# Kernel tuning notes

Measured on AMD Instinct MI355X. Metric: run time of the kernel, lower is better.

## Reference

```python
import jax, jax.numpy as jnp
import numpy as np
import math

B, S = 512, 100
L, U = 50000, 2000
D, LOC_DIM, USER_DIM, TEMP_DIM = 80, 56, 12, 12
NHEAD, DFF = 4, 160


def _pe(seq_len, d):
    pos = np.arange(seq_len, dtype=np.float32)[:, None]
    div = np.exp(np.arange(0, d, 2, dtype=np.float32) * (-math.log(10000.0) / d))
    pe = np.zeros((seq_len, d), dtype=np.float32)
    pe[:, 0::2] = np.sin(pos * div)
    pe[:, 1::2] = np.cos(pos * div)
    return jnp.asarray(pe)


def _ln(x, g, b, eps=1e-5):
    m = x.mean(-1, keepdims=True)
    v = ((x - m) ** 2).mean(-1, keepdims=True)
    return (x - m) * jax.lax.rsqrt(v + eps) * g + b


def setup_inputs():
    key = jax.random.key(0)
    ks = jax.random.split(key, 16)
    f32 = jnp.float32
    def n(k, shape, s):
        return (jax.random.normal(k, shape) * s).astype(f32)
    return {
        'loc_seq': jax.random.randint(ks[0], (B, S), 0, L),
        'user_seq': jax.random.randint(ks[1], (B, S), 0, U),
        'weekday_seq': jax.random.randint(ks[2], (B, S), 0, 7),
        'start_min_seq': (jax.random.uniform(ks[3], (B, S)) * 1440.0).astype(f32),
        'dur_seq': (jax.random.uniform(ks[4], (B, S)) * 120.0).astype(f32),
        'diff_seq': jax.random.randint(ks[5], (B, S), 0, 7),
        'mask': jnp.ones((B, S), dtype=bool),
        'loc_emb': n(ks[6], (L, LOC_DIM), 0.01).at[0].set(0.0),
        'user_emb': n(ks[7], (U, USER_DIM), 0.01).at[0].set(0.0),
        'Wt': n(ks[8], (6, TEMP_DIM), 0.3), 'bt': jnp.zeros((TEMP_DIM,), f32),
        'in_g': jnp.ones((D,), f32), 'in_b': jnp.zeros((D,), f32),
        'Wq': n(ks[9], (D, D), 0.05), 'bq': jnp.zeros((D,), f32),
        'Wk': n(ks[10], (D, D), 0.05), 'bk': jnp.zeros((D,), f32),
        'Wv': n(ks[11], (D, D), 0.05), 'bv': jnp.zeros((D,), f32),
        'Wo': n(ks[12], (D, D), 0.05), 'bo': jnp.zeros((D,), f32),
        'ln1_g': jnp.ones((D,), f32), 'ln1_b': jnp.zeros((D,), f32),
        'W1': n(ks[13], (D, DFF), 0.05), 'b1': jnp.zeros((DFF,), f32),
        'W2': n(ks[14], (DFF, D), 0.05), 'b2': jnp.zeros((D,), f32),
        'ln2_g': jnp.ones((D,), f32), 'ln2_b': jnp.zeros((D,), f32),
        'out_g': jnp.ones((D,), f32), 'out_b': jnp.zeros((D,), f32),
        'Wp': n(ks[15], (D, L), 0.05), 'bp': jnp.zeros((L,), f32),
        'recency_decay': jnp.array(0.62, f32),
        'freq_weight': jnp.array(2.2, f32),
        'history_scale': jnp.array(11.0, f32),
        'model_weight': jnp.array(0.22, f32),
    }


def reference(loc_seq, user_seq, weekday_seq, start_min_seq, dur_seq, diff_seq, mask,
              loc_emb, user_emb, Wt, bt, in_g, in_b,
              Wq, bq, Wk, bk, Wv, bv, Wo, bo, ln1_g, ln1_b,
              W1, b1, W2, b2, ln2_g, ln2_b, out_g, out_b, Wp, bp,
              recency_decay, freq_weight, history_scale, model_weight):
    b, s = loc_seq.shape
    nloc = Wp.shape[1]
    valid = mask.astype(jnp.float32)
    # --- history scores: the torch per-timestep scatter loop, vectorized ---
    t = jnp.arange(s)
    rec_w = recency_decay ** (s - 1 - t).astype(jnp.float32)      # (s,) decay^time_from_end
    bidx = jnp.broadcast_to(jnp.arange(b)[:, None], (b, s))
    recency = jnp.zeros((b, nloc), jnp.float32).at[bidx, loc_seq].max(rec_w[None, :] * valid)
    freq = jnp.zeros((b, nloc), jnp.float32).at[bidx, loc_seq].add(valid)
    freq = freq / jnp.maximum(freq.max(axis=1, keepdims=True), 1.0)
    history_scores = history_scale * (recency + freq_weight * freq)
    # --- embeddings & temporal features ---
    time_rad = start_min_seq / 60.0 / 24.0 * 2.0 * math.pi
    wd_rad = weekday_seq.astype(jnp.float32) / 7.0 * 2.0 * math.pi
    feats = jnp.stack([jnp.sin(time_rad), jnp.cos(time_rad), jnp.log1p(dur_seq) / 8.0,
                       jnp.sin(wd_rad), jnp.cos(wd_rad), diff_seq.astype(jnp.float32) / 7.0], axis=-1)
    x = jnp.concatenate([loc_emb[loc_seq], user_emb[user_seq], feats @ Wt + bt], axis=-1)
    x = _ln(x, in_g, in_b) + _pe(s, x.shape[-1])[None]
    # --- 1-layer post-norm transformer encoder, erf-gelu, eval (no dropout) ---
    dh = D // NHEAD
    q = (x @ Wq + bq).reshape(b, s, NHEAD, dh)
    k = (x @ Wk + bk).reshape(b, s, NHEAD, dh)
    v = (x @ Wv + bv).reshape(b, s, NHEAD, dh)
    scores = jnp.einsum('bqhd,bkhd->bhqk', q, k) / math.sqrt(dh)
    scores = jnp.where(mask[:, None, None, :], scores, -1e9)
    attn = jnp.einsum('bhqk,bkhd->bqhd', jax.nn.softmax(scores, axis=-1), v).reshape(b, s, D)
    x = _ln(x + attn @ Wo + bo, ln1_g, ln1_b)
    x = _ln(x + jax.nn.gelu(x @ W1 + b1, approximate=False) @ W2 + b2, ln2_g, ln2_b)
    # --- gather last valid position ---
    last_idx = mask.sum(axis=1) - 1
    last = jnp.take_along_axis(x, last_idx[:, None, None], axis=1)[:, 0]
    last = _ln(last, out_g, out_b)
    learned = jax.nn.softmax(last @ Wp + bp, axis=1) * nloc
    return history_scores + model_weight * learned
```

## Files before the change

kernel.cpp:

```cpp
#include <hip/hip_runtime.h>
#include <hip/hip_bf16.h>
#include <math.h>

#define B 512
#define S 100
#define L 50000
#define D 80
#define NHEAD 4
#define DH 20
#define DFF 160
#define NTOK (B*S)
#define NTILES 3125

typedef __attribute__((ext_vector_type(8))) short bf16x8v;
typedef __attribute__((ext_vector_type(4))) float f32x4v;
typedef __attribute__((ext_vector_type(4))) unsigned short u16x4;
typedef __attribute__((ext_vector_type(8))) unsigned short u16x8;

__device__ __forceinline__ unsigned short f2bf(float f) {
    unsigned int x = __float_as_uint(f);
    unsigned int r = (x + 0x7FFFu + ((x >> 16) & 1u)) >> 16;
    return (unsigned short)r;
}

__device__ __forceinline__ float bf2f(unsigned short u) {
    return __uint_as_float(((unsigned int)u) << 16);
}

__device__ __forceinline__ float pe_val(int s, int d) {
    int k = d >> 1;
    float ang = (float)s * expf(-0.23025850929940458f * (float)k);
    return (d & 1) ? cosf(ang) : sinf(ang);
}

__global__ __launch_bounds__(256) void pack_all(const float* __restrict__ Wq, const float* __restrict__ Wk,
                        const float* __restrict__ Wv, const float* __restrict__ Wo,
                        const float* __restrict__ W1, const float* __restrict__ W2,
                        unsigned short* __restrict__ U) {
    int bid = blockIdx.x;
    const float* W; int K, N, KT, nt; unsigned short* dst;
    if (bid < 15)      { int mt = bid / 5; nt = bid % 5; W = (mt==0)?Wq:(mt==1)?Wk:Wv; K=80; N=80; KT=3; dst = U + (size_t)bid * 1536; }
    else if (bid < 20) { nt = bid - 15; W = Wo; K=80;  N=80;  KT=3; dst = U + 23040 + (size_t)nt * 1536; }
    else if (bid < 30) { nt = bid - 20; W = W1; K=80;  N=160; KT=3; dst = U + 30720 + (size_t)nt * 1536; }
    else               { nt = bid - 30; W = W2; K=160; N=80;  KT=5; dst = U + 46080 + (size_t)nt * 2560; }
    int total = KT * 512;
    for (int idx = threadIdx.x; idx < total; idx += 256) {
        int j = idx & 7, n = (idx >> 3) & 15, q = (idx >> 7) & 3, kt = idx >> 9;
        int k = kt * 32 + q * 8 + j;
        float val = (k < K) ? W[(size_t)k * N + nt * 16 + n] : 0.f;
        dst[idx] = f2bf(val);
    }
}

__global__ __launch_bounds__(256) void build_x(const int* __restrict__ loc_seq, const int* __restrict__ user_seq,
                        const int* __restrict__ weekday_seq, const float* __restrict__ start_min,
                        const float* __restrict__ dur, const int* __restrict__ diff,
                        const float* __restrict__ loc_emb, const float* __restrict__ user_emb,
                        const float* __restrict__ Wt, const float* __restrict__ bt,
                        const float* __restrict__ in_g, const float* __restrict__ in_b,
                        unsigned short* __restrict__ x) {
    int token = blockIdx.x * 4 + (threadIdx.x >> 6);
    int lane = threadIdx.x & 63;
    int s = token % S;
    int lidx = loc_seq[token];
    int uidx = user_seq[token];
    float tr = start_min[token] * (2.f * (float)M_PI / 1440.f);
    float wd = (float)weekday_seq[token] * (2.f * (float)M_PI / 7.f);
    float f0 = sinf(tr), f1 = cosf(tr);
    float f2 = log1pf(dur[token]) * 0.125f;
    float f3 = sinf(wd), f4 = cosf(wd);
    float f5 = (float)diff[token] * (1.f / 7.f);
    float v1;
    if (lane < 56) v1 = loc_emb[(size_t)lidx * 56 + lane];
    else           v1 = user_emb[(size_t)uidx * 12 + (lane - 56)];
    float v2 = 0.f;
    if (lane < 4) {
        v2 = user_emb[(size_t)uidx * 12 + 8 + lane];
    } else if (lane < 16) {
        int j = lane - 4;
        v2 = bt[j] + f0 * Wt[j] + f1 * Wt[12 + j] + f2 * Wt[24 + j]
                   + f3 * Wt[36 + j] + f4 * Wt[48 + j] + f5 * Wt[60 + j];
    }
    float sum = v1 + v2, sq = v1 * v1 + v2 * v2;
    #pragma unroll
    for (int off = 1; off < 64; off <<= 1) {
        sum += __shfl_xor(sum, off);
        sq  += __shfl_xor(sq,  off);
    }
    float mean = sum * 0.0125f;
    float var = sq * 0.0125f - mean * mean;
    float rstd = rsqrtf(var + 1e-5f);
    x[(size_t)token * D + lane] = f2bf((v1 - mean) * rstd * in_g[lane] + in_b[lane] + pe_val(s, lane));
    if (lane < 16) {
        int d2 = 64 + lane;
        x[(size_t)token * D + d2] = f2bf((v2 - mean) * rstd * in_g[d2] + in_b[d2] + pe_val(s, d2));
    }
}

__global__ __launch_bounds__(512) void qkv_attn_fused(const unsigned short* __restrict__ xg,
      const unsigned short* __restrict__ qkvP,
      const float* __restrict__ bq, const float* __restrict__ bk, const float* __restrict__ bv,
      unsigned short* __restrict__ ao) {
    __shared__ __align__(16) unsigned short qls[128 * 128];
    __shared__ __align__(16) unsigned short kls[112 * 128];
    __shared__ __align__(16) unsigned short vt[4 * 32 * 128];
    __shared__ __align__(16) unsigned short pqk[128 * 128];
    int tid = threadIdx.x;
    int b = blockIdx.x;
    unsigned short* xbf = pqk;
    size_t base = (size_t)b * (S * D);
    f32x4v zz = {0.f, 0.f, 0.f, 0.f};
    f32x4v* q4 = (f32x4v*)qls; f32x4v* k4 = (f32x4v*)kls; f32x4v* v4 = (f32x4v*)vt;
    #pragma unroll
    for (int ii = 0; ii < 4; ++ii) q4[tid + ii * 512] = zz;
    #pragma unroll
    for (int ii = 0; ii < 4; ++ii) { int i = tid + ii * 512; if (i < 1792) k4[i] = zz; }
    #pragma unroll
    for (int ii = 0; ii < 4; ++ii) v4[tid + ii * 512] = zz;
    #pragma unroll
    for (int ii = 0; ii < 4; ++ii) {
        int i = tid + ii * 512;
        if (i < 2000) {
            int row = i / 20, c0 = (i % 20) * 4;
            *(u16x4*)&xbf[row * 96 + c0] = *(const u16x4*)&xg[base + row * 80 + c0];
        }
    }
    unsigned int* xb32 = (unsigned int*)xbf;
    for (int i = tid; i < 576; i += 512) xb32[4800 + i] = 0;
    for (int i = tid; i < 800; i += 512) { int r = i / 8, c = i % 8; xb32[r * 48 + 40 + c] = 0; }
    __syncthreads();
    int w = tid >> 6, lane = tid & 63;
    int qd = lane >> 4, m = lane & 15;
    if (w < 7) {
        int mt = w;
        bf16x8v a[3];
        #pragma unroll
        for (int t = 0; t < 3; ++t)
            a[t] = *(const bf16x8v*)&xbf[(mt * 16 + m) * 96 + t * 32 + qd * 8];
        #pragma unroll
        for (int nt = 0; nt < 15; ++nt) {
            f32x4v acc = {0.f, 0.f, 0.f, 0.f};
            #pragma unroll
            for (int t = 0; t < 3; ++t) {
                bf16x8v bb = *(const bf16x8v*)&qkvP[(((size_t)(nt * 3 + t)) * 4 + qd) * 128 + m * 8];
                acc = __builtin_amdgcn_mfma_f32_16x16x32_bf16(a[t], bb, acc, 0, 0, 0);
            }
            int mat = nt / 5;
            int col80 = nt * 16 + m - mat * 80;
            int h = col80 / 20, dd = col80 % 20;
            const float* bias = (mat == 0) ? bq : (mat == 1) ? bk : bv;
            float bbv = bias[col80];
            float scl = (mat == 0) ? 0.22360679774997896f : 1.f;
            #pragma unroll
            for (int r = 0; r < 4; ++r) {
                int row = mt * 16 + qd * 4 + r;
                unsigned short val = f2bf((acc[r] + bbv) * scl);
                if (mat == 0)      qls[row * 128 + ((h * 32 + dd) ^ ((row & 7) << 3))] = val;
                else if (mat == 1) kls[row * 128 + ((h * 32 + dd) ^ ((row & 7) << 3))] = val;
                else               vt[h * 4096 + dd * 128 + (row ^ ((dd & 7) << 3))] = val;
            }
        }
    }
    __syncthreads();
    {
        int i = tid;
        int row = i >> 2, j = (i & 3) * 4;
        u16x4 zp = {0, 0, 0, 0};
        *(u16x4*)&pqk[row * 128 + ((112 + j) ^ ((row & 7) << 3))] = zp;
    }
    f32x4v os[4][2];
    #pragma unroll
    for (int h = 0; h < 4; ++h) {
        int hb = h * 32;
        int rowq = w * 16 + m;
        bf16x8v aq = *(const bf16x8v*)&qls[rowq * 128 + ((hb + qd * 8) ^ ((rowq & 7) << 3))];
        f32x4v sc[7];
        #pragma unroll
        for (int nt = 0; nt < 7; ++nt) {
            int krow = nt * 16 + m;
            bf16x8v bk_ = *(const bf16x8v*)&kls[krow * 128 + ((hb + qd * 8) ^ ((krow & 7) << 3))];
            f32x4v z = {0.f, 0.f, 0.f, 0.f};
            sc[nt] = __builtin_amdgcn_mfma_f32_16x16x32_bf16(aq, bk_, z, 0, 0, 0);
        }
        float inv_l[4];
        #pragma unroll
        for (int r = 0; r < 4; ++r) {
            float mx = sc[0][r];
            #pragma unroll
            for (int nt = 1; nt < 6; ++nt) mx = fmaxf(mx, sc[nt][r]);
            float s6 = sc[6][r];
            if (m < 4) mx = fmaxf(mx, s6);
            #pragma unroll
            for (int off = 1; off < 16; off <<= 1) mx = fmaxf(mx, __shfl_xor(mx, off));
            float l = 0.f;
            #pragma unroll
            for (int nt = 0; nt < 6; ++nt) {
                float p = expf(sc[nt][r] - mx);
                sc[nt][r] = p; l += p;
            }
            float p6 = (m < 4) ? expf(s6 - mx) : 0.f;
            sc[6][r] = p6; l += p6;
            #pragma unroll
            for (int off = 1; off < 16; off <<= 1) l += __shfl_xor(l, off);
            inv_l[r] = 1.f / l;
        }
        __syncthreads();
        #pragma unroll
        for (int r = 0; r < 4; ++r) {
            int row = w * 16 + qd * 4 + r;
            int sw = (row & 7) << 3;
            #pragma unroll
            for (int nt = 0; nt < 7; ++nt)
                pqk[row * 128 + ((nt * 16 + m) ^ sw)] = f2bf(sc[nt][r]);
        }
        __syncthreads();
        #pragma unroll
        for (int nt2 = 0; nt2 < 2; ++nt2) { f32x4v z = {0.f,0.f,0.f,0.f}; os[h][nt2] = z; }
        #pragma unroll
        for (int kt = 0; kt < 4; ++kt) {
            int ksw = (m & 7) << 3;
            bf16x8v bv0 = *(const bf16x8v*)&vt[h * 4096 + (m) * 128 + ((kt * 32 + qd * 8) ^ ksw)];
            bf16x8v bv1 = *(const bf16x8v*)&vt[h * 4096 + (16 + m) * 128 + ((kt * 32 + qd * 8) ^ ksw)];
            int row = w * 16 + m;
            bf16x8v pa = *(const bf16x8v*)&pqk[row * 128 + ((kt * 32 + qd * 8) ^ ksw)];
            os[h][0] = __builtin_amdgcn_mfma_f32_16x16x32_bf16(pa, bv0, os[h][0], 0, 0, 0);
            os[h][1] = __builtin_amdgcn_mfma_f32_16x16x32_bf16(pa, bv1, os[h][1], 0, 0, 0);
        }
        #pragma unroll
        for (int r = 0; r < 4; ++r) {
            os[h][0][r] *= inv_l[r];
            os[h][1][r] *= inv_l[r];
        }
    }
    __syncthreads();
    unsigned short* aols = pqk;
    #pragma unroll
    for (int h = 0; h < 4; ++h) {
        #pragma unroll
        for (int r = 0; r < 4; ++r) {
            int row = w * 16 + qd * 4 + r;
            aols[row * 96 + h * 20 + m] = f2bf(os[h][0][r]);
            if (m < 4) aols[row * 96 + h * 20 + 16 + m] = f2bf(os[h][1][r]);
        }
    }
    __syncthreads();
    #pragma unroll
    for (int ii = 0; ii < 2; ++ii) {
        int i = tid + ii * 512;
        if (i < 1000) {
            int row = i / 10, c = (i % 10) * 8;
            *(u16x8*)&ao[base + row * 80 + c] = *(u16x8*)&aols[row * 96 + c];
        }
    }
}

__global__ __launch_bounds__(256) void encoder_tail(const unsigned short* __restrict__ aog,
      const unsigned short* __restrict__ xg,
      const unsigned short* __restrict__ woP, const float* __restrict__ bo,
      const float* __restrict__ ln1g, const float* __restrict__ ln1b,
      const unsigned short* __restrict__ w1P, const float* __restrict__ b1,
      const unsigned short* __restrict__ w2P, const float* __restrict__ b2,
      const float* __restrict__ ln2g, const float* __restrict__ ln2b,
      const float* __restrict__ outg, const float* __restrict__ outb,
      unsigned short* __restrict__ apack) {
    __shared__ unsigned short ubuf[64 * 160];
    __shared__ unsigned short xbf[64 * 96];
    __shared__ float ys[64 * 84];
    __shared__ float rsum[64][4], rsq[64][4];
    __shared__ float mstat[64], rstat[64];
    int tid = threadIdx.x;
    size_t base = (size_t)blockIdx.x * 64 * D;
    #pragma unroll
    for (int ii = 0; ii < 5; ++ii) {
        int i = tid + ii * 256;
        int row = i / 20, c0 = (i % 20) * 4;
        *(u16x4*)&ubuf[row * 96 + c0] = *(const u16x4*)&aog[base + row * 80 + c0];
        u16x4 xv = *(const u16x4*)&xg[base + row * 80 + c0];
        f32x4v xf;
        #pragma unroll
        for (int j = 0; j < 4; ++j) xf[j] = bf2f(xv[j]);
        *(f32x4v*)&ys[row * 84 + c0] = xf;
    }
    #pragma unroll
    for (int ii = 0; ii < 2; ++ii) {
        int i = tid + ii * 256;
        int row = i >> 3, c = i & 7;
        ((unsigned int*)ubuf)[row * 48 + 40 + c] = 0;
    }
    __syncthreads();
    int w = tid >> 6, lane = tid & 63;
    int qd = lane >> 4, m = lane & 15;
    {
        bf16x8v a[3];
        #pragma unroll
        for (int t = 0; t < 3; ++t)
            a[t] = *(const bf16x8v*)&ubuf[(w * 16 + m) * 96 + t * 32 + qd * 8];
        #pragma unroll
        for (int nt = 0; nt < 5; ++nt) {
            f32x4v acc = {0.f, 0.f, 0.f, 0.f};
            #pragma unroll
            for (int t = 0; t < 3; ++t) {
                bf16x8v b = *(const bf16x8v*)&woP[(((size_t)(nt * 3 + t)) * 4 + qd) * 128 + m * 8];
                acc = __builtin_amdgcn_mfma_f32_16x16x32_bf16(a[t], b, acc, 0, 0, 0);
            }
            int col = nt * 16 + m;
            float bbv = bo[col];
            #pragma unroll
            for (int r = 0; r < 4; ++r)
                ys[(w * 16 + qd * 4 + r) * 84 + col] += acc[r] + bbv;
        }
    }
    __syncthreads();
    {
        int row = tid >> 2, qq = tid & 3;
        float s = 0.f, sq = 0.f;
        #pragma unroll
        for (int j = 0; j < 20; ++j) { float v = ys[row * 84 + qq + 4 * j]; s += v; sq += v * v; }
        rsum[row][qq] = s; rsq[row][qq] = sq;
    }
    __syncthreads();
    if (tid < 64) {
        float s = rsum[tid][0] + rsum[tid][1] + rsum[tid][2] + rsum[tid][3];
        float sq = rsq[tid][0] + rsq[tid][1] + rsq[tid][2] + rsq[tid][3];
        float mean = s * 0.0125f;
        float var = sq * 0.0125f - mean * mean;
        mstat[tid] = mean; rstat[tid] = rsqrtf(var + 1e-5f);
    }
    __syncthreads();
    for (int idx = tid; idx < 64 * 96; idx += 256) {
        int row = idx / 96, kk = idx % 96;
        float val = 0.f;
        if (kk < D) {
            val = (ys[row * 84 + kk] - mstat[row]) * rstat[row] * ln1g[kk] + ln1b[kk];
            ys[row * 84 + kk] = val;
        }
        xbf[idx] = f2bf(val);
    }
    __syncthreads();
    {
        bf16x8v a[3];
        #pragma unroll
        for (int t = 0; t < 3; ++t)
            a[t] = *(const bf16x8v*)&xbf[(w * 16 + m) * 96 + t * 32 + qd * 8];
        #pragma unroll
        for (int nt = 0; nt < 10; ++nt) {
            f32x4v acc = {0.f, 0.f, 0.f, 0.f};
            #pragma unroll
            for (int t = 0; t < 3; ++t) {
                bf16x8v b = *(const bf16x8v*)&w1P[(((size_t)(nt * 3 + t)) * 4 + qd) * 128 + m * 8];
                acc = __builtin_amdgcn_mfma_f32_16x16x32_bf16(a[t], b, acc, 0, 0, 0);
            }
            int col = nt * 16 + m;
            float bbv = b1[col];
            #pragma unroll
            for (int r = 0; r < 4; ++r) {
                float aa = acc[r] + bbv;
                float gl = 0.5f * aa * (1.f + erff(aa * 0.70710678118654752f));
                ubuf[(w * 16 + qd * 4 + r) * 160 + col] = f2bf(gl);
            }
        }
    }
    __syncthreads();
    {
        bf16x8v a2[5];
        #pragma unroll
        for (int t = 0; t < 5; ++t)
            a2[t] = *(const bf16x8v*)&ubuf[(w * 16 + m) * 160 + t * 32 + qd * 8];
        #pragma unroll
        for (int nt = 0; nt < 5; ++nt) {
            f32x4v acc = {0.f, 0.f, 0.f, 0.f};
            #pragma unroll
            for (int t = 0; t < 5; ++t) {
                bf16x8v b = *(const bf16x8v*)&w2P[(((size_t)(nt * 5 + t)) * 4 + qd) * 128 + m * 8];
                acc = __builtin_amdgcn_mfma_f32_16x16x32_bf16(a2[t], b, acc, 0, 0, 0);
            }
            int col = nt * 16 + m;
            float bbv = b2[col];
            #pragma unroll
            for (int r = 0; r < 4; ++r)
                ys[(w * 16 + qd * 4 + r) * 84 + col] += acc[r] + bbv;
        }
    }
    __syncthreads();
    {
        int row = tid >> 2, qq = tid & 3;
        float s = 0.f, sq = 0.f;
        #pragma unroll
        for (int j = 0; j < 20; ++j) { float v = ys[row * 84 + qq + 4 * j]; s += v; sq += v * v; }
        rsum[row][qq] = s; rsq[row][qq] = sq;
    }
    __syncthreads();
    if (tid < 64) {
        float s = rsum[tid][0] + rsum[tid][1] + rsum[tid][2] + rsum[tid][3];
        float sq = rsq[tid][0] + rsq[tid][1] + rsq[tid][2] + rsq[tid][3];
        float mean = s * 0.0125f;
        float var = sq * 0.0125f - mean * mean;
        mstat[tid] = mean; rstat[tid] = rsqrtf(var + 1e-5f);
    }
    __syncthreads();
    int t0 = blockIdx.x * 64;
    int srow = (99 - (t0 % 100)) % 100;
    if (srow < 64) {
        float* lastrow = (float*)rsum;
        if (tid < 80)
            lastrow[tid] = (ys[srow * 84 + tid] - mstat[srow]) * rstat[srow] * ln2g[tid] + ln2b[tid];
        __syncthreads();
        if (tid < 64) {
            float v1 = lastrow[tid];
            float v2 = (tid < 16) ? lastrow[64 + tid] : 0.f;
            float sum = v1 + v2, sq = v1 * v1 + v2 * v2;
            #pragma unroll
            for (int off = 1; off < 64; off <<= 1) {
                sum += __shfl_xor(sum, off);
                sq  += __shfl_xor(sq,  off);
            }
            float mean = sum * 0.0125f;
            float var = sq * 0.0125f - mean * mean;
            float rstd = rsqrtf(var + 1e-5f);
            int bb = (t0 + srow) / 100;
            int mtile = bb >> 4, mm = bb & 15;
            {
                int d = tid;
                float val = (v1 - mean) * rstd * outg[d] + outb[d];
                int t = d >> 5, q = (d & 31) >> 3, j = d & 7;
                apack[((((size_t)mtile * 3 + t) * 4 + q) * 16 + mm) * 8 + j] = f2bf(val);
            }
            if (tid < 32) {
                int d = 64 + tid;
                float val = (tid < 16) ? ((v2 - mean) * rstd * outg[d] + outb[d]) : 0.f;
                int t = d >> 5, q = (d & 31) >> 3, j = d & 7;
                apack[((((size_t)mtile * 3 + t) * 4 + q) * 16 + mm) * 8 + j] = f2bf(val);
            }
        }
    }
}

__global__ __launch_bounds__(256) void wp_pack(const float* __restrict__ Wp, unsigned short* __restrict__ bpack,
                                               float* __restrict__ rowsum) {
    int tid = threadIdx.x;
    int nt = blockIdx.x;
    if (nt == 0) { rowsum[tid] = 0.f; rowsum[256 + tid] = 0.f; }
    for (int idx = tid; idx < 1536; idx += 256) {
        int n = idx & 15, kk = idx >> 4;
        int t = kk >> 5, q = (kk & 31) >> 3, j = kk & 7;
        float val = (kk < D) ? Wp[(size_t)kk * L + nt * 16 + n] : 0.f;
        bpack[((((size_t)nt * 3 + t) * 4 + q) * 16 + n) * 8 + j] = f2bf(val);
    }
}

__global__ __launch_bounds__(256) void rowsum_mfma(const unsigned short* __restrict__ apack,
                                                   const unsigned short* __restrict__ bpack,
                                                   const float* __restrict__ bp,
                                                   float* __restrict__ rowsum) {
    __shared__ float part[4][512];
    int tid = threadIdx.x;
    int w = tid >> 6, lane = tid & 63;
    int q = lane >> 4, m = lane & 15;
    int nt0 = (blockIdx.x * 4 + w) * 4;
    const bf16x8v* BP = (const bf16x8v*)bpack;
    const bf16x8v* AP = (const bf16x8v*)apack;
    bf16x8v bfr[4][3];
    float bpv[4], liv[4];
    #pragma unroll
    for (int i = 0; i < 4; ++i) {
        int ntile = nt0 + i;
        int ntc = ntile < NTILES ? ntile : NTILES - 1;
        liv[i] = ntile < NTILES ? 1.f : 0.f;
        #pragma unroll
        for (int t = 0; t < 3; ++t)
            bfr[i][t] = BP[((size_t)ntc * 3 + t) * 64 + q * 16 + m];
        bpv[i] = bp[ntc * 16 + m];
    }
    for (int mt = 0; mt < 32; ++mt) {
        bf16x8v a[3];
        #pragma unroll
        for (int t = 0; t < 3; ++t) a[t] = AP[((size_t)mt * 3 + t) * 64 + q * 16 + m];
        float rs[4] = {0.f, 0.f, 0.f, 0.f};
        #pragma unroll
        for (int i = 0; i < 4; ++i) {
            f32x4v acc = {0.f, 0.f, 0.f, 0.f};
            #pragma unroll
            for (int t = 0; t < 3; ++t)
                acc = __builtin_amdgcn_mfma_f32_16x16x32_bf16(a[t], bfr[i][t], acc, 0, 0, 0);
            #pragma unroll
            for (int r = 0; r < 4; ++r) rs[r] += liv[i] * expf(acc[r] + bpv[i]);
        }
        #pragma unroll
        for (int r = 0; r < 4; ++r) {
            #pragma unroll
            for (int off = 1; off < 16; off <<= 1) rs[r] += __shfl_xor(rs[r], off);
        }
        if (m == 0) {
            #pragma unroll
            for (int r = 0; r < 4; ++r) part[w][mt * 16 + q * 4 + r] = rs[r];
        }
    }
    __syncthreads();
    for (int i = tid; i < 512; i += 256) {
        float s = part[0][i] + part[1][i] + part[2][i] + part[3][i];
        atomicAdd(&rowsum[i], s);
    }
}

__global__ __launch_bounds__(256) void logits_final(const unsigned short* __restrict__ apack,
      const unsigned short* __restrict__ bpack, const float* __restrict__ bp,
      const float* __restrict__ rowsum, const float* __restrict__ mwp,
      float* __restrict__ out) {
    __shared__ float tile[2][16][68];
    __shared__ float sc[512];
    int tid = threadIdx.x;
    int w = tid >> 6, lane = tid & 63;
    int q = lane >> 4, m = lane & 15;
    float mwL = mwp[0] * (float)L;
    for (int i = tid; i < 512; i += 256) sc[i] = mwL / rowsum[i];
    int ntile = blockIdx.x * 4 + w;
    int ntc = ntile < NTILES ? ntile : NTILES - 1;
    bool live = ntile < NTILES;
    const bf16x8v* BP = (const bf16x8v*)bpack;
    const bf16x8v* AP = (const bf16x8v*)apack;
    bf16x8v bfr[3];
    #pragma unroll
    for (int t = 0; t < 3; ++t) bfr[t] = BP[((size_t)ntc * 3 + t) * 64 + q * 16 + m];
    float bpv = bp[ntc * 16 + m];
    int row = tid >> 4, c4 = tid & 15;
    int gc = blockIdx.x * 64 + c4 * 4;
    bool cok = gc + 4 <= L;
    bf16x8v aC[3], aN[3];
    #pragma unroll
    for (int t = 0; t < 3; ++t) aC[t] = AP[(size_t)t * 64 + q * 16 + m];
    __syncthreads();
    for (int mt = 0; mt < 32; ++mt) {
        if (mt < 31) {
            #pragma unroll
            for (int t = 0; t < 3; ++t) aN[t] = AP[((size_t)(mt + 1) * 3 + t) * 64 + q * 16 + m];
        }
        f32x4v acc = {0.f, 0.f, 0.f, 0.f};
        #pragma unroll
        for (int t = 0; t < 3; ++t)
            acc = __builtin_amdgcn_mfma_f32_16x16x32_bf16(aC[t], bfr[t], acc, 0, 0, 0);
        int buf = mt & 1;
        if (live) {
            #pragma unroll
            for (int r = 0; r < 4; ++r)
                tile[buf][q * 4 + r][w * 16 + m] = expf(acc[r] + bpv);
        }
        __syncthreads();
        if (cok) {
            float4 v = *(float4*)&tile[buf][row][c4 * 4];
            float s = sc[mt * 16 + row];
            v.x *= s; v.y *= s; v.z *= s; v.w *= s;
            *(float4*)&out[(size_t)(mt * 16 + row) * L + gc] = v;
        }
        #pragma unroll
        for (int t = 0; t < 3; ++t) aC[t] = aN[t];
    }
}

__global__ void history_kern(const int* __restrict__ loc_seq, const float* __restrict__ decp,
                             const float* __restrict__ fwp, const float* __restrict__ hsp,
                             float* __restrict__ out) {
    int b = blockIdx.x;
    int t = threadIdx.x;
    __shared__ int locs[S];
    __shared__ float red[128];
    if (t < S) locs[t] = loc_seq[(size_t)b * S + t];
    __syncthreads();
    int cnt = 0;
    bool isLast = false;
    int myloc = -1;
    if (t < S) {
        myloc = locs[t];
        isLast = true;
        for (int u = 0; u < S; ++u) {
            if (locs[u] == myloc) { cnt++; if (u > t) isLast = false; }
        }
    }
    red[t] = (float)cnt;
    __syncthreads();
    for (int off = 64; off; off >>= 1) { if (t < off) red[t] = fmaxf(red[t], red[t + off]); __syncthreads(); }
    float denom = fmaxf(red[0], 1.0f);
    if (t < S && isLast) {
        float rec = powf(decp[0], (float)(S - 1 - t));
        out[(size_t)b * L + myloc] += hsp[0] * (rec + fwp[0] * (float)cnt / denom);
    }
}

extern "C" void kernel_launch(void* const* d_in, const int* in_sizes, int n_in,
                              void* d_out, int out_size, void* d_ws, size_t ws_size,
                              hipStream_t stream) {
    (void)in_sizes; (void)n_in; (void)out_size; (void)ws_size;
    const int*   loc_seq   = (const int*)  d_in[0];
    const int*   user_seq  = (const int*)  d_in[1];
    const int*   weekday   = (const int*)  d_in[2];
    const float* start_min = (const float*)d_in[3];
    const float* dur       = (const float*)d_in[4];
    const int*   diff      = (const int*)  d_in[5];
    const float* loc_emb = (const float*)d_in[7];
    const float* user_emb= (const float*)d_in[8];
    const float* Wt  = (const float*)d_in[9];  const float* bt  = (const float*)d_in[10];
    const float* in_g= (const float*)d_in[11]; const float* in_b= (const float*)d_in[12];
    const float* Wq  = (const float*)d_in[13]; const float* bq  = (const float*)d_in[14];
    const float* Wk  = (const float*)d_in[15]; const float* bk  = (const float*)d_in[16];
    const float* Wv  = (const float*)d_in[17]; const float* bv  = (const float*)d_in[18];
    const float* Wo  = (const float*)d_in[19]; const float* bo  = (const float*)d_in[20];
    const float* ln1g= (const float*)d_in[21]; const float* ln1b= (const float*)d_in[22];
    const float* W1  = (const float*)d_in[23]; const float* b1  = (const float*)d_in[24];
    const float* W2  = (const float*)d_in[25]; const float* b2  = (const float*)d_in[26];
    const float* ln2g= (const float*)d_in[27]; const float* ln2b= (const float*)d_in[28];
    const float* outg= (const float*)d_in[29]; const float* outb= (const float*)d_in[30];
    const float* Wp  = (const float*)d_in[31]; const float* bp  = (const float*)d_in[32];
    const float* dec = (const float*)d_in[33]; const float* fw  = (const float*)d_in[34];
    const float* hs  = (const float*)d_in[35]; const float* mw  = (const float*)d_in[36];

    float* ws   = (float*)d_ws;
    unsigned short* Xb = (unsigned short*)ws;
    unsigned short* APACK = (unsigned short*)(ws + 4096000);
    unsigned short* AO = (unsigned short*)(ws + 16384000);
    float* RSUM = ws + 20480000;
    unsigned short* WPACKS = (unsigned short*)(ws + 20481000);
    unsigned short* QKVP = WPACKS;
    unsigned short* WOP  = WPACKS + 23040;
    unsigned short* W1P  = WPACKS + 30720;
    unsigned short* W2P  = WPACKS + 46080;
    unsigned short* BPACK = AO;
    float* out  = (float*)d_out;

    pack_all<<<35, 256, 0, stream>>>(Wq, Wk, Wv, Wo, W1, W2, WPACKS);
    build_x<<<NTOK / 4, 256, 0, stream>>>(loc_seq, user_seq, weekday, start_min, dur, diff,
                                          loc_emb, user_emb, Wt, bt, in_g, in_b, Xb);
    qkv_attn_fused<<<B, 512, 0, stream>>>(Xb, QKVP, bq, bk, bv, AO);
    encoder_tail<<<NTOK / 64, 256, 0, stream>>>(AO, Xb, WOP, bo, ln1g, ln1b,
                                                W1P, b1, W2P, b2, ln2g, ln2b,
                                                outg, outb, APACK);
    wp_pack<<<NTILES, 256, 0, stream>>>(Wp, BPACK, RSUM);
    rowsum_mfma<<<(NTILES + 15) / 16, 256, 0, stream>>>(APACK, BPACK, bp, RSUM);
    logits_final<<<(NTILES + 3) / 4, 256, 0, stream>>>(APACK, BPACK, bp, RSUM, mw, out);
    history_kern<<<B, 128, 0, stream>>>(loc_seq, dec, fw, hs, out);
}
```

Measured before the change: 372.3 us.

## Compute attention and encoder tail only for the last sequence position

```diff
diff --git a/kernel.cpp b/kernel.cpp
--- a/kernel.cpp
+++ b/kernel.cpp
@@ -97,26 +97,26 @@
     }
 }
 
-__global__ __launch_bounds__(512) void qkv_attn_fused(const unsigned short* __restrict__ xg,
+__global__ __launch_bounds__(512) void qkv_attn_last(const unsigned short* __restrict__ xg,
       const unsigned short* __restrict__ qkvP,
       const float* __restrict__ bq, const float* __restrict__ bk, const float* __restrict__ bv,
-      unsigned short* __restrict__ ao) {
-    __shared__ __align__(16) unsigned short qls[128 * 128];
+      unsigned short* __restrict__ ao_last) {
+    __shared__ __align__(16) unsigned short xbf[112 * 96];
     __shared__ __align__(16) unsigned short kls[112 * 128];
     __shared__ __align__(16) unsigned short vt[4 * 32 * 128];
-    __shared__ __align__(16) unsigned short pqk[128 * 128];
+    __shared__ __align__(16) unsigned short qls[16 * 128];
+    __shared__ float pls[4 * 112];
+    __shared__ float lls[4];
     int tid = threadIdx.x;
     int b = blockIdx.x;
-    unsigned short* xbf = pqk;
     size_t base = (size_t)b * (S * D);
     f32x4v zz = {0.f, 0.f, 0.f, 0.f};
-    f32x4v* q4 = (f32x4v*)qls; f32x4v* k4 = (f32x4v*)kls; f32x4v* v4 = (f32x4v*)vt;
-    #pragma unroll
-    for (int ii = 0; ii < 4; ++ii) q4[tid + ii * 512] = zz;
+    f32x4v* k4 = (f32x4v*)kls; f32x4v* v4 = (f32x4v*)vt; f32x4v* q4 = (f32x4v*)qls;
     #pragma unroll
     for (int ii = 0; ii < 4; ++ii) { int i = tid + ii * 512; if (i < 1792) k4[i] = zz; }
     #pragma unroll
     for (int ii = 0; ii < 4; ++ii) v4[tid + ii * 512] = zz;
+    if (tid < 256) q4[tid] = zz;
     #pragma unroll
     for (int ii = 0; ii < 4; ++ii) {
         int i = tid + ii * 512;
@@ -155,106 +155,60 @@
             for (int r = 0; r < 4; ++r) {
                 int row = mt * 16 + qd * 4 + r;
                 unsigned short val = f2bf((acc[r] + bbv) * scl);
-                if (mat == 0)      qls[row * 128 + ((h * 32 + dd) ^ ((row & 7) << 3))] = val;
-                else if (mat == 1) kls[row * 128 + ((h * 32 + dd) ^ ((row & 7) << 3))] = val;
-                else               vt[h * 4096 + dd * 128 + (row ^ ((dd & 7) << 3))] = val;
+                if (mat == 0) {
+                    if (row >= 96) qls[(row - 96) * 128 + ((h * 32 + dd) ^ ((row & 7) << 3))] = val;
+                } else if (mat == 1) {
+                    kls[row * 128 + ((h * 32 + dd) ^ ((row & 7) << 3))] = val;
+                } else {
+                    vt[h * 4096 + dd * 128 + (row ^ ((dd & 7) << 3))] = val;
+                }
             }
         }
     }
     __syncthreads();
-    {
-        int i = tid;
-        int row = i >> 2, j = (i & 3) * 4;
-        u16x4 zp = {0, 0, 0, 0};
-        *(u16x4*)&pqk[row * 128 + ((112 + j) ^ ((row & 7) << 3))] = zp;
-    }
-    f32x4v os[4][2];
-    #pragma unroll
-    for (int h = 0; h < 4; ++h) {
-        int hb = h * 32;
-        int rowq = w * 16 + m;
-        bf16x8v aq = *(const bf16x8v*)&qls[rowq * 128 + ((hb + qd * 8) ^ ((rowq & 7) << 3))];
-        f32x4v sc[7];
+    if (w < 4) {
+        int hb = w * 32;
+        bf16x8v aq = *(const bf16x8v*)&qls[m * 128 + ((hb + qd * 8) ^ ((m & 7) << 3))];
+        f32x4v scv[7];
         #pragma unroll
         for (int nt = 0; nt < 7; ++nt) {
             int krow = nt * 16 + m;
             bf16x8v bk_ = *(const bf16x8v*)&kls[krow * 128 + ((hb + qd * 8) ^ ((krow & 7) << 3))];
             f32x4v z = {0.f, 0.f, 0.f, 0.f};
-            sc[nt] = __builtin_amdgcn_mfma_f32_16x16x32_bf16(aq, bk_, z, 0, 0, 0);
-        }
-        float inv_l[4];
-        #pragma unroll
-        for (int r = 0; r < 4; ++r) {
-            float mx = sc[0][r];
-            #pragma unroll
-            for (int nt = 1; nt < 6; ++nt) mx = fmaxf(mx, sc[nt][r]);
-            float s6 = sc[6][r];
-            if (m < 4) mx = fmaxf(mx, s6);
-            #pragma unroll
-            for (int off = 1; off < 16; off <<= 1) mx = fmaxf(mx, __shfl_xor(mx, off));
-            float l = 0.f;
-            #pragma unroll
-            for (int nt = 0; nt < 6; ++nt) {
-                float p = expf(sc[nt][r] - mx);
-                sc[nt][r] = p; l += p;
-            }
-            float p6 = (m < 4) ? expf(s6 - mx) : 0.f;
-            sc[6][r] = p6; l += p6;
-            #pragma unroll
-            for (int off = 1; off < 16; off <<= 1) l += __shfl_xor(l, off);
-            inv_l[r] = 1.f / l;
-        }
-        __syncthreads();
-        #pragma unroll
-        for (int r = 0; r < 4; ++r) {
-            int row = w * 16 + qd * 4 + r;
-            int sw = (row & 7) << 3;
-            #pragma unroll
-            for (int nt = 0; nt < 7; ++nt)
-                pqk[row * 128 + ((nt * 16 + m) ^ sw)] = f2bf(sc[nt][r]);
-        }
-        __syncthreads();
-        #pragma unroll
-        for (int nt2 = 0; nt2 < 2; ++nt2) { f32x4v z = {0.f,0.f,0.f,0.f}; os[h][nt2] = z; }
-        #pragma unroll
-        for (int kt = 0; kt < 4; ++kt) {
-            int ksw = (m & 7) << 3;
-            bf16x8v bv0 = *(const bf16x8v*)&vt[h * 4096 + (m) * 128 + ((kt * 32 + qd * 8) ^ ksw)];
-            bf16x8v bv1 = *(const bf16x8v*)&vt[h * 4096 + (16 + m) * 128 + ((kt * 32 + qd * 8) ^ ksw)];
-            int row = w * 16 + m;
-            bf16x8v pa = *(const bf16x8v*)&pqk[row * 128 + ((kt * 32 + qd * 8) ^ ksw)];
-            os[h][0] = __builtin_amdgcn_mfma_f32_16x16x32_bf16(pa, bv0, os[h][0], 0, 0, 0);
-            os[h][1] = __builtin_amdgcn_mfma_f32_16x16x32_bf16(pa, bv1, os[h][1], 0, 0, 0);
-        }
-        #pragma unroll
-        for (int r = 0; r < 4; ++r) {
-            os[h][0][r] *= inv_l[r];
-            os[h][1][r] *= inv_l[r];
-        }
-    }
-    __syncthreads();
-    unsigned short* aols = pqk;
-    #pragma unroll
-    for (int h = 0; h < 4; ++h) {
-        #pragma unroll
-        for (int r = 0; r < 4; ++r) {
-            int row = w * 16 + qd * 4 + r;
-            aols[row * 96 + h * 20 + m] = f2bf(os[h][0][r]);
-            if (m < 4) aols[row * 96 + h * 20 + 16 + m] = f2bf(os[h][1][r]);
-        }
-    }
-    __syncthreads();
-    #pragma unroll
-    for (int ii = 0; ii < 2; ++ii) {
-        int i = tid + ii * 512;
-        if (i < 1000) {
-            int row = i / 10, c = (i % 10) * 8;
-            *(u16x8*)&ao[base + row * 80 + c] = *(u16x8*)&aols[row * 96 + c];
-        }
-    }
-}
-
-__global__ __launch_bounds__(256) void encoder_tail(const unsigned short* __restrict__ aog,
+            scv[nt] = __builtin_amdgcn_mfma_f32_16x16x32_bf16(aq, bk_, z, 0, 0, 0);
+        }
+        float mx = scv[0][3];
+        #pragma unroll
+        for (int nt = 1; nt < 6; ++nt) mx = fmaxf(mx, scv[nt][3]);
+        float s6 = scv[6][3];
+        if (m < 4) mx = fmaxf(mx, s6);
+        #pragma unroll
+        for (int off = 1; off < 16; off <<= 1) mx = fmaxf(mx, __shfl_xor(mx, off));
+        float p[7], l = 0.f;
+        #pragma unroll
+        for (int nt = 0; nt < 6; ++nt) { p[nt] = expf(scv[nt][3] - mx); l += p[nt]; }
+        p[6] = (m < 4) ? expf(s6 - mx) : 0.f; l += p[6];
+        #pragma unroll
+        for (int off = 1; off < 16; off <<= 1) l += __shfl_xor(l, off);
+        if (qd == 0) {
+            #pragma unroll
+            for (int nt = 0; nt < 7; ++nt) pls[w * 112 + nt * 16 + m] = p[nt];
+            if (m == 0) lls[w] = l;
+        }
+    }
+    __syncthreads();
+    if (w < 4 && lane < 20) {
+        float invl = 1.f / lls[w];
+        int dsw = (lane & 7) << 3;
+        float acc = 0.f;
+        #pragma unroll 4
+        for (int s = 0; s < 100; ++s)
+            acc += pls[w * 112 + s] * bf2f(vt[w * 4096 + lane * 128 + (s ^ dsw)]);
+        ao_last[(size_t)b * 80 + w * 20 + lane] = f2bf(acc * invl);
+    }
+}
+
+__global__ __launch_bounds__(256) void tail_kern(const unsigned short* __restrict__ ao_last,
       const unsigned short* __restrict__ xg,
       const unsigned short* __restrict__ woP, const float* __restrict__ bo,
       const float* __restrict__ ln1g, const float* __restrict__ ln1b,
@@ -269,13 +223,13 @@
     __shared__ float rsum[64][4], rsq[64][4];
     __shared__ float mstat[64], rstat[64];
     int tid = threadIdx.x;
-    size_t base = (size_t)blockIdx.x * 64 * D;
+    int b0 = blockIdx.x * 64;
     #pragma unroll
     for (int ii = 0; ii < 5; ++ii) {
         int i = tid + ii * 256;
         int row = i / 20, c0 = (i % 20) * 4;
-        *(u16x4*)&ubuf[row * 96 + c0] = *(const u16x4*)&aog[base + row * 80 + c0];
-        u16x4 xv = *(const u16x4*)&xg[base + row * 80 + c0];
+        *(u16x4*)&ubuf[row * 96 + c0] = *(const u16x4*)&ao_last[(size_t)(b0 + row) * 80 + c0];
+        u16x4 xv = *(const u16x4*)&xg[((size_t)(b0 + row) * S + (S - 1)) * 80 + c0];
         f32x4v xf;
         #pragma unroll
         for (int j = 0; j < 4; ++j) xf[j] = bf2f(xv[j]);
@@ -398,40 +352,35 @@
         mstat[tid] = mean; rstat[tid] = rsqrtf(var + 1e-5f);
     }
     __syncthreads();
-    int t0 = blockIdx.x * 64;
-    int srow = (99 - (t0 % 100)) % 100;
-    if (srow < 64) {
-        float* lastrow = (float*)rsum;
-        if (tid < 80)
-            lastrow[tid] = (ys[srow * 84 + tid] - mstat[srow]) * rstat[srow] * ln2g[tid] + ln2b[tid];
-        __syncthreads();
-        if (tid < 64) {
-            float v1 = lastrow[tid];
-            float v2 = (tid < 16) ? lastrow[64 + tid] : 0.f;
-            float sum = v1 + v2, sq = v1 * v1 + v2 * v2;
-            #pragma unroll
-            for (int off = 1; off < 64; off <<= 1) {
-                sum += __shfl_xor(sum, off);
-                sq  += __shfl_xor(sq,  off);
-            }
-            float mean = sum * 0.0125f;
-            float var = sq * 0.0125f - mean * mean;
-            float rstd = rsqrtf(var + 1e-5f);
-            int bb = (t0 + srow) / 100;
-            int mtile = bb >> 4, mm = bb & 15;
-            {
-                int d = tid;
-                float val = (v1 - mean) * rstd * outg[d] + outb[d];
-                int t = d >> 5, q = (d & 31) >> 3, j = d & 7;
-                apack[((((size_t)mtile * 3 + t) * 4 + q) * 16 + mm) * 8 + j] = f2bf(val);
-            }
-            if (tid < 32) {
-                int d = 64 + tid;
-                float val = (tid < 16) ? ((v2 - mean) * rstd * outg[d] + outb[d]) : 0.f;
-                int t = d >> 5, q = (d & 31) >> 3, j = d & 7;
-                apack[((((size_t)mtile * 3 + t) * 4 + q) * 16 + mm) * 8 + j] = f2bf(val);
-            }
-        }
+    for (int idx = tid; idx < 64 * 80; idx += 256) {
+        int row = idx / 80, col = idx % 80;
+        ys[row * 84 + col] = (ys[row * 84 + col] - mstat[row]) * rstat[row] * ln2g[col] + ln2b[col];
+    }
+    __syncthreads();
+    {
+        int row = tid >> 2, qq = tid & 3;
+        float s = 0.f, sq = 0.f;
+        #pragma unroll
+        for (int j = 0; j < 20; ++j) { float v = ys[row * 84 + qq + 4 * j]; s += v; sq += v * v; }
+        rsum[row][qq] = s; rsq[row][qq] = sq;
+    }
+    __syncthreads();
+    if (tid < 64) {
+        float s = rsum[tid][0] + rsum[tid][1] + rsum[tid][2] + rsum[tid][3];
+        float sq = rsq[tid][0] + rsq[tid][1] + rsq[tid][2] + rsq[tid][3];
+        float mean = s * 0.0125f;
+        float var = sq * 0.0125f - mean * mean;
+        mstat[tid] = mean; rstat[tid] = rsqrtf(var + 1e-5f);
+    }
+    __syncthreads();
+    for (int idx = tid; idx < 64 * 96; idx += 256) {
+        int row = idx / 96, d = idx % 96;
+        float val = 0.f;
+        if (d < 80) val = (ys[row * 84 + d] - mstat[row]) * rstat[row] * outg[d] + outb[d];
+        int bb = b0 + row;
+        int mtile = bb >> 4, mm = bb & 15;
+        int t = d >> 5, q = (d & 31) >> 3, j = d & 7;
+        apack[((((size_t)mtile * 3 + t) * 4 + q) * 16 + mm) * 8 + j] = f2bf(val);
     }
 }
 
@@ -615,23 +564,23 @@
     float* ws   = (float*)d_ws;
     unsigned short* Xb = (unsigned short*)ws;
     unsigned short* APACK = (unsigned short*)(ws + 4096000);
-    unsigned short* AO = (unsigned short*)(ws + 16384000);
     float* RSUM = ws + 20480000;
     unsigned short* WPACKS = (unsigned short*)(ws + 20481000);
     unsigned short* QKVP = WPACKS;
     unsigned short* WOP  = WPACKS + 23040;
     unsigned short* W1P  = WPACKS + 30720;
     unsigned short* W2P  = WPACKS + 46080;
-    unsigned short* BPACK = AO;
+    unsigned short* AOL  = WPACKS + 60000;
+    unsigned short* BPACK = (unsigned short*)(ws + 16384000);
     float* out  = (float*)d_out;
 
     pack_all<<<35, 256, 0, stream>>>(Wq, Wk, Wv, Wo, W1, W2, WPACKS);
     build_x<<<NTOK / 4, 256, 0, stream>>>(loc_seq, user_seq, weekday, start_min, dur, diff,
                                           loc_emb, user_emb, Wt, bt, in_g, in_b, Xb);
-    qkv_attn_fused<<<B, 512, 0, stream>>>(Xb, QKVP, bq, bk, bv, AO);
-    encoder_tail<<<NTOK / 64, 256, 0, stream>>>(AO, Xb, WOP, bo, ln1g, ln1b,
-                                                W1P, b1, W2P, b2, ln2g, ln2b,
-                                                outg, outb, APACK);
+    qkv_attn_last<<<B, 512, 0, stream>>>(Xb, QKVP, bq, bk, bv, AOL);
+    tail_kern<<<B / 64, 256, 0, stream>>>(AOL, Xb, WOP, bo, ln1g, ln1b,
+                                          W1P, b1, W2P, b2, ln2g, ln2b,
+                                          outg, outb, APACK);
     wp_pack<<<NTILES, 256, 0, stream>>>(Wp, BPACK, RSUM);
     rowsum_mfma<<<(NTILES + 15) / 16, 256, 0, stream>>>(APACK, BPACK, bp, RSUM);
     logits_final<<<(NTILES + 3) / 4, 256, 0, stream>>>(APACK, BPACK, bp, RSUM, mw, out);
```

Result: faster. 343.0 us (-7.9%).
